# Kernel tuning notes

Hardware: AMD Instinct MI355X
Metric: run time of the kernel (lower is better)

Reference implementation:

```python
import jax, jax.numpy as jnp
import numpy as np

D_MODEL = 1024
N_HEADS = 16
D_K = D_MODEL // N_HEADS
THETA = 10000.0
B, S = 4, 2048


def setup_inputs() -> dict:
    key = jax.random.key(0)
    ks = jax.random.split(key, 5)
    scale = 0.02
    return {
        "x": jax.random.normal(ks[0], (B, S, D_MODEL), dtype=jnp.float32),
        "token_positions": jnp.arange(S, dtype=jnp.int32),
        "WQ": jax.random.normal(ks[1], (D_MODEL, D_MODEL), dtype=jnp.float32) * scale,
        "WK": jax.random.normal(ks[2], (D_MODEL, D_MODEL), dtype=jnp.float32) * scale,
        "WV": jax.random.normal(ks[3], (D_MODEL, D_MODEL), dtype=jnp.float32) * scale,
        "WO": jax.random.normal(ks[4], (D_MODEL, D_MODEL), dtype=jnp.float32) * scale,
    }


def apply_rope(x, positions):
    # x: [B, H, S, d_k]; rotate interleaved (even, odd) pairs
    half = D_K // 2
    inv_freq = THETA ** (-jnp.arange(half, dtype=x.dtype) * 2.0 / D_K)  # [half]
    ang = positions.astype(x.dtype)[:, None] * inv_freq[None, :]        # [S, half]
    cos, sin = jnp.cos(ang), jnp.sin(ang)
    x1 = x[..., 0::2]
    x2 = x[..., 1::2]
    r1 = x1 * cos - x2 * sin
    r2 = x1 * sin + x2 * cos
    return jnp.stack([r1, r2], axis=-1).reshape(x.shape)


def reference(x, token_positions, WQ, WK, WV, WO):
    b, s, _ = x.shape
    # Linear (no bias), weight stored (out, in): y = x @ W^T
    def proj(W):
        y = jnp.einsum('bsd,ed->bse', x, W)
        return y.reshape(b, s, N_HEADS, D_K).transpose(0, 2, 1, 3)  # [b,h,s,dk]
    Q, K, V = proj(WQ), proj(WK), proj(WV)
    Q = apply_rope(Q, token_positions)
    K = apply_rope(K, token_positions)
    scores = jnp.einsum('bhqd,bhkd->bhqk', Q, K) / jnp.sqrt(jnp.asarray(D_K, x.dtype))
    causal = jnp.tril(jnp.ones((s, s), dtype=bool))
    scores = jnp.where(causal, scores, -jnp.inf)
    attn = jax.nn.softmax(scores, axis=-1)
    out = jnp.einsum('bhqk,bhkd->bhqd', attn, V)
    out = out.transpose(0, 2, 1, 3).reshape(b, s, D_MODEL)
    return jnp.einsum('bse,de->bsd', out, WO)
```

## Files before the change

kernel.cpp:

```cpp
#include <hip/hip_runtime.h>
#include <cstdint>
#include <cstddef>

#define DM 1024
#define NH 16
#define DKD 64
#define BB 4
#define SS 2048
#define MTOT (BB*SS)

typedef float  f32x4  __attribute__((ext_vector_type(4)));
typedef __bf16 bf16x8 __attribute__((ext_vector_type(8)));
typedef __bf16 bf16x4v __attribute__((ext_vector_type(4)));
typedef __bf16 bf16x2v __attribute__((ext_vector_type(2)));
using as3v = __attribute__((address_space(3))) void;
using as1v = __attribute__((address_space(1))) void;

__device__ __forceinline__ void gl2lds16(const void* g, void* l) {
  __builtin_amdgcn_global_load_lds((as1v*)g, (as3v*)l, 16, 0, 0);
}

__device__ __forceinline__ float fast_exp2(float x) {
#if __has_builtin(__builtin_amdgcn_exp2f)
  return __builtin_amdgcn_exp2f(x);
#else
  return __expf(x * 0.6931471805599453f);
#endif
}

__device__ __forceinline__ void sincos_rev(float rev, float* s, float* c) {
#if __has_builtin(__builtin_amdgcn_sinf) && __has_builtin(__builtin_amdgcn_cosf)
  *s = __builtin_amdgcn_sinf(rev);
  *c = __builtin_amdgcn_cosf(rev);
#else
  float a = rev * 6.283185307179586f;
  *s = __sinf(a); *c = __cosf(a);
#endif
}

__device__ __forceinline__ uint32_t pkbf(float a, float b) {
  union { uint32_t u; __bf16 h[2]; } c;
  c.h[0] = (__bf16)a; c.h[1] = (__bf16)b;
  return c.u;
}

__global__ void cast_all_k(const float* __restrict__ x,
                           const float* __restrict__ wq, const float* __restrict__ wk,
                           const float* __restrict__ wv, const float* __restrict__ wo,
                           __bf16* __restrict__ xb,
                           __bf16* __restrict__ wqb, __bf16* __restrict__ wkb,
                           __bf16* __restrict__ wvb, __bf16* __restrict__ wob) {
  int i = blockIdx.x * blockDim.x + threadIdx.x;
  const float* src;
  __bf16* dst;
  int idx, oidx;
  if (i < 2097152) {
    src = x; dst = xb; idx = i; oidx = i;
  } else {
    int j = i - 2097152;
    int w = j >> 18;
    idx = j & 262143;
    src = (w == 0) ? wq : (w == 1) ? wk : (w == 2) ? wv : wo;
    dst = (w == 0) ? wqb : (w == 1) ? wkb : (w == 2) ? wvb : wob;
    if (w < 2) {
      int e = idx >> 8;
      int c = idx & 255;
      int d = e & 63;
      int dp = (d & 1) ? 32 + (d >> 1) : (d >> 1);
      oidx = (((e & ~63) | dp) << 8) | c;
    } else {
      oidx = idx;
    }
  }
  float4 f = ((const float4*)src)[idx];
  bf16x4v o;
  o[0] = (__bf16)f.x; o[1] = (__bf16)f.y; o[2] = (__bf16)f.z; o[3] = (__bf16)f.w;
  ((bf16x4v*)dst)[oidx] = o;
}

__global__ void rope_tbl_k(const int* __restrict__ pos, float2* __restrict__ tbl) {
  int p = blockIdx.x * blockDim.x + threadIdx.x;
  int s = p >> 5;
  int i = p & 31;
  float ps = (float)pos[s];
  float invr = __expf(-0.28782313663f * (float)i) * 0.15915494309f;
  float rev = ps * invr;
  rev -= floorf(rev);
  float sn, cs;
  sincos_rev(rev, &sn, &cs);
  tbl[p] = make_float2(cs, sn);
}

template <typename CT>
__global__ __launch_bounds__(256) void gemm_bt_k(const __bf16* __restrict__ A,
                                                 const __bf16* __restrict__ B,
                                                 CT* __restrict__ C,
                                                 int M, int N, int K) {
  __shared__ __bf16 As[128 * 32];
  __shared__ __bf16 Bs[128 * 32];
  const int tid  = threadIdx.x;
  const int lane = tid & 63;
  const int wid  = tid >> 6;
  const int lrow = lane & 15;
  const int quad = lane >> 4;
  const int m0 = blockIdx.y * 128;
  const int n0 = blockIdx.x * 128;
  const int wm = (wid & 1) * 64;
  const int wn = (wid >> 1) * 64;
  const int srow = wid * 32 + (lane >> 2);
  const int scol = (lane & 3) * 8;

  f32x4 acc[4][4] = {};

  for (int k0 = 0; k0 < K; k0 += 32) {
    __syncthreads();
    gl2lds16(A + (size_t)(m0 + srow)      * K + k0 + scol, As + (wid * 32)      * 32);
    gl2lds16(A + (size_t)(m0 + srow + 16) * K + k0 + scol, As + (wid * 32 + 16) * 32);
    gl2lds16(B + (size_t)(n0 + srow)      * K + k0 + scol, Bs + (wid * 32)      * 32);
    gl2lds16(B + (size_t)(n0 + srow + 16) * K + k0 + scol, Bs + (wid * 32 + 16) * 32);
    __syncthreads();

    bf16x8 af[4], bfr[4];
#pragma unroll
    for (int i = 0; i < 4; ++i)
      af[i] = *(const bf16x8*)(As + (wm + i * 16 + lrow) * 32 + quad * 8);
#pragma unroll
    for (int i = 0; i < 4; ++i)
      bfr[i] = *(const bf16x8*)(Bs + (wn + i * 16 + lrow) * 32 + quad * 8);
#pragma unroll
    for (int mi = 0; mi < 4; ++mi)
#pragma unroll
      for (int ni = 0; ni < 4; ++ni)
        acc[mi][ni] = __builtin_amdgcn_mfma_f32_16x16x32_bf16(af[mi], bfr[ni], acc[mi][ni], 0, 0, 0);
  }

#pragma unroll
  for (int mi = 0; mi < 4; ++mi)
#pragma unroll
    for (int ni = 0; ni < 4; ++ni)
#pragma unroll
      for (int r = 0; r < 4; ++r) {
        int row = m0 + wm + mi * 16 + quad * 4 + r;
        int col = n0 + wn + ni * 16 + lrow;
        C[(size_t)row * N + col] = (CT)acc[mi][ni][r];
      }
}

__global__ __launch_bounds__(256) void gemm_qkv_k(const __bf16* __restrict__ A,
                                                  const __bf16* __restrict__ Bq,
                                                  const __bf16* __restrict__ Bk,
                                                  const __bf16* __restrict__ Bv,
                                                  const float2* __restrict__ tbl,
                                                  __bf16* __restrict__ Cq,
                                                  __bf16* __restrict__ Ck,
                                                  __bf16* __restrict__ Cv) {
  __shared__ __bf16 As[128 * 32];
  __shared__ __bf16 Bs[128 * 32];
  const int sel = blockIdx.x >> 3;
  const __bf16* B = sel == 0 ? Bq : sel == 1 ? Bk : Bv;
  const int n0 = (blockIdx.x & 7) * 128;
  const int m0 = blockIdx.y * 128;
  const int K = DM;
  const int tid  = threadIdx.x;
  const int lane = tid & 63;
  const int wid  = tid >> 6;
  const int lrow = lane & 15;
  const int quad = lane >> 4;
  const int wm = (wid & 1) * 64;
  const int wn = (wid >> 1) * 64;
  const int srow = wid * 32 + (lane >> 2);
  const int scol = (lane & 3) * 8;

  f32x4 acc[4][4] = {};

  for (int k0 = 0; k0 < K; k0 += 32) {
    __syncthreads();
    gl2lds16(A + (size_t)(m0 + srow)      * K + k0 + scol, As + (wid * 32)      * 32);
    gl2lds16(A + (size_t)(m0 + srow + 16) * K + k0 + scol, As + (wid * 32 + 16) * 32);
    gl2lds16(B + (size_t)(n0 + srow)      * K + k0 + scol, Bs + (wid * 32)      * 32);
    gl2lds16(B + (size_t)(n0 + srow + 16) * K + k0 + scol, Bs + (wid * 32 + 16) * 32);
    __syncthreads();

    bf16x8 af[4], bfr[4];
#pragma unroll
    for (int i = 0; i < 4; ++i)
      af[i] = *(const bf16x8*)(As + (wm + i * 16 + lrow) * 32 + quad * 8);
#pragma unroll
    for (int i = 0; i < 4; ++i)
      bfr[i] = *(const bf16x8*)(Bs + (wn + i * 16 + lrow) * 32 + quad * 8);
#pragma unroll
    for (int mi = 0; mi < 4; ++mi)
#pragma unroll
      for (int ni = 0; ni < 4; ++ni)
        acc[mi][ni] = __builtin_amdgcn_mfma_f32_16x16x32_bf16(af[mi], bfr[ni], acc[mi][ni], 0, 0, 0);
  }

  const int hbase = (n0 + wn) >> 6;
  const int bq = m0 >> 11;

  if (sel == 2) {
    __bf16* vt = Cv + ((size_t)(bq * NH + hbase)) * (DKD * SS);
    const int S0 = (m0 + wm) & (SS - 1);
#pragma unroll
    for (int ni = 0; ni < 4; ++ni) {
      const int d = ni * 16 + lrow;
#pragma unroll
      for (int mi = 0; mi < 4; ++mi) {
        bf16x4v pk;
#pragma unroll
        for (int r = 0; r < 4; ++r) pk[r] = (__bf16)acc[mi][ni][r];
        const int sp = S0 + (mi >> 1) * 32 + quad * 8 + (mi & 1) * 4;
        *(bf16x4v*)(vt + (size_t)d * SS + sp) = pk;
      }
    }
  } else {
    __bf16* C = ((sel == 0) ? Cq : Ck) + ((size_t)(bq * NH + hbase)) * (SS * DKD);
#pragma unroll
    for (int ni = 0; ni < 2; ++ni) {
      const int i = ni * 16 + lrow;
#pragma unroll
      for (int mi = 0; mi < 4; ++mi) {
#pragma unroll
        for (int r = 0; r < 4; ++r) {
          int s = (m0 + wm + mi * 16 + quad * 4 + r) & (SS - 1);
          float2 cssn = tbl[s * 32 + i];
          float a = acc[mi][ni][r];
          float b = acc[mi][ni + 2][r];
          C[(size_t)s * DKD + i]      = (__bf16)fmaf(a, cssn.x, -(b * cssn.y));
          C[(size_t)s * DKD + 32 + i] = (__bf16)fmaf(a, cssn.y,  (b * cssn.x));
        }
      }
    }
  }
}

__global__ __launch_bounds__(512, 4) void attn10_k(const __bf16* __restrict__ Qh,
                                                   const __bf16* __restrict__ Kh,
                                                   const __bf16* __restrict__ VT,
                                                   __bf16* __restrict__ O) {
  __shared__ __bf16 Ks[2][128 * 64];
  __shared__ __bf16 Vt[2][64 * 128];
  const int tid  = threadIdx.x;
  const int lane = tid & 63;
  const int wid  = tid >> 6;
  const int lrow = lane & 15;
  const int quad = lane >> 4;
  const int j   = blockIdx.x;
  const int xcd = j & 7;
  const int t   = j >> 3;
  const int bh  = (xcd << 3) | (t >> 3);
  const int pr  = t & 7;
  const int qa  = pr;
  const int qb  = 15 - pr;
  const int na  = qa + 1;
  const int b  = bh >> 4;
  const int h  = bh & 15;
  const size_t hb = (size_t)bh * (SS * DKD);

  const int skr = lane >> 3;
  const int skc = lane & 7;
  const int svd = lane >> 4;
  const int svc = lane & 15;

  auto stage = [&](int kt, int bsel) {
#pragma unroll
    for (int ii = 0; ii < 2; ++ii) {
      int i = wid * 2 + ii;
      int key = i * 8 + skr;
      int gc = skc ^ (key & 7);
      gl2lds16(Kh + hb + (size_t)(kt * 128 + key) * DKD + gc * 8, &Ks[bsel][i * 512]);
      int dk = i * 4 + svd;
      int gc2 = (svc & 8) | ((svc ^ dk) & 7);
      gl2lds16(VT + hb + (size_t)dk * SS + kt * 128 + gc2 * 8, &Vt[bsel][i * 512]);
    }
  };

  stage(0, 0);
  int it = 0;

  for (int seg = 0; seg < 2; ++seg) {
    const int qi  = seg ? qb : qa;
    const int q0  = qi * 128;
    const int nkt = qi + 1;
    const int qg  = q0 + wid * 16 + lrow;

    bf16x8 qf0, qf1;
    {
      const __bf16* qp = Qh + hb + (size_t)qg * DKD + quad * 8;
      qf0 = *(const bf16x8*)qp;
      qf1 = *(const bf16x8*)(qp + 32);
    }
    f32x4 Oa[4] = {};
    float la = 0.f, lb = 0.f;

    for (int kt = 0; kt < nkt; ++kt, ++it) {
      __syncthreads();
      {
        int nit = it + 1;
        if (nit < 17) {
          int nk = (nit < na) ? nit : (nit - na);
          stage(nk, nit & 1);
        }
      }
      const __bf16* ks = Ks[it & 1];
      const __bf16* vt = Vt[it & 1];

      f32x4 sa[8];
#pragma unroll
      for (int mi = 0; mi < 8; ++mi) sa[mi] = (f32x4){0.f, 0.f, 0.f, 0.f};
      __builtin_amdgcn_s_setprio(1);
#pragma unroll
      for (int tt = 0; tt < 2; ++tt) {
        bf16x8 qf = tt ? qf1 : qf0;
#pragma unroll
        for (int mi = 0; mi < 8; ++mi) {
          bf16x8 kf = *(const bf16x8*)(ks + (mi * 16 + lrow) * 64 + (((tt * 4 + quad) ^ (lrow & 7)) * 8));
          sa[mi] = __builtin_amdgcn_mfma_f32_16x16x32_bf16(kf, qf, sa[mi], 0, 0, 0);
        }
      }
      __builtin_amdgcn_s_setprio(0);

      const bool lastt = (kt == nkt - 1);
#pragma unroll
      for (int kc = 0; kc < 4; ++kc) {
        union { uint32_t u[4]; bf16x8 v; } P;
#pragma unroll
        for (int half = 0; half < 2; ++half) {
          const int mi = kc * 2 + half;
          float pr4[4];
#pragma unroll
          for (int r = 0; r < 4; ++r) {
            float p = fast_exp2(sa[mi][r] * 0.18033688f - 8.0f);
            if (lastt) {
              int key = kt * 128 + kc * 32 + half * 16 + quad * 4 + r;
              p = (key <= qg) ? p : 0.f;
            }
            pr4[r] = p;
          }
          float s01 = pr4[0] + pr4[1];
          float s23 = pr4[2] + pr4[3];
          if (half) lb += (s01 + s23); else la += (s01 + s23);
          P.u[half * 2]     = pkbf(pr4[0], pr4[1]);
          P.u[half * 2 + 1] = pkbf(pr4[2], pr4[3]);
        }
        __builtin_amdgcn_s_setprio(1);
#pragma unroll
        for (int ni = 0; ni < 4; ++ni) {
          int c = kc * 4 + quad;
          int cp = (c & 8) | ((c ^ (lrow & 7)) & 7);
          bf16x8 vf = *(const bf16x8*)(vt + (ni * 16 + lrow) * 128 + cp * 8);
          Oa[ni] = __builtin_amdgcn_mfma_f32_16x16x32_bf16(P.v, vf, Oa[ni], 0, 0, 0);
        }
        __builtin_amdgcn_s_setprio(0);
      }
    }

    float l = la + lb;
    l += __shfl_xor(l, 16, 64);
    l += __shfl_xor(l, 32, 64);
#pragma unroll
    for (int r = 0; r < 4; ++r) {
      float li = __shfl(l, quad * 4 + r, 64);
      float inv = 1.0f / li;
      int row = q0 + wid * 16 + quad * 4 + r;
#pragma unroll
      for (int ni = 0; ni < 4; ++ni)
        O[(size_t)b * SS * DM + (size_t)row * DM + h * DKD + ni * 16 + lrow] =
            (__bf16)(Oa[ni][r] * inv);
    }
  }
}

extern "C" void kernel_launch(void* const* d_in, const int* in_sizes, int n_in,
                              void* d_out, int out_size, void* d_ws, size_t ws_size,
                              hipStream_t stream) {
  (void)in_sizes; (void)n_in; (void)out_size; (void)ws_size;
  const float* x  = (const float*)d_in[0];
  const int*   pos = (const int*)d_in[1];
  const float* WQ = (const float*)d_in[2];
  const float* WK = (const float*)d_in[3];
  const float* WV = (const float*)d_in[4];
  const float* WO = (const float*)d_in[5];
  float* out = (float*)d_out;

  char* w = (char*)d_ws;
  const size_t MB = 1024 * 1024;
  __bf16* xb  = (__bf16*)(w);
  __bf16* wqb = (__bf16*)(w + 16 * MB);
  __bf16* wkb = (__bf16*)(w + 18 * MB);
  __bf16* wvb = (__bf16*)(w + 20 * MB);
  __bf16* wob = (__bf16*)(w + 22 * MB);
  __bf16* Qh  = (__bf16*)(w + 24 * MB);
  __bf16* Kh  = (__bf16*)(w + 40 * MB);
  __bf16* Cb  = (__bf16*)(w + 56 * MB);
  __bf16* VT  = (__bf16*)(w + 72 * MB);
  float2* tbl = (float2*)(w + 88 * MB);

  cast_all_k<<<3145728 / 256, 256, 0, stream>>>(x, WQ, WK, WV, WO, xb, wqb, wkb, wvb, wob);

  rope_tbl_k<<<(SS * 32) / 256, 256, 0, stream>>>(pos, tbl);

  gemm_qkv_k<<<dim3(24, MTOT / 128), 256, 0, stream>>>(xb, wqb, wkb, wvb, tbl, Qh, Kh, VT);

  attn10_k<<<dim3(512), 512, 0, stream>>>(Qh, Kh, VT, Cb);

  gemm_bt_k<float><<<dim3(DM / 128, MTOT / 128), 256, 0, stream>>>(Cb, wob, out, MTOT, DM, DM);
}
```

Before: 256.1 us.

## Double-buffer LDS tiles with XOR swizzle and MFMA priority in GEMM kernels

Both the generic GEMM and the fused QKV GEMM now keep two LDS buffers. The next K-tile's global-to-LDS loads are issued right after a single barrier, so they overlap the MFMA work on the current tile instead of stalling behind two barriers per iteration. The LDS tile layout is XOR-swizzled across pairs of rows to cut bank conflicts on the fragment reads. s_setprio is raised around the MFMA block, and launch bounds request 4 blocks per SM. The trade-off is double the LDS footprint per block and more index arithmetic, which could limit occupancy.

```diff
diff --git a/kernel.cpp b/kernel.cpp
--- a/kernel.cpp
+++ b/kernel.cpp
@@ -91,13 +91,14 @@
   tbl[p] = make_float2(cs, sn);
 }
 
+
 template <typename CT>
-__global__ __launch_bounds__(256) void gemm_bt_k(const __bf16* __restrict__ A,
-                                                 const __bf16* __restrict__ B,
-                                                 CT* __restrict__ C,
-                                                 int M, int N, int K) {
-  __shared__ __bf16 As[128 * 32];
-  __shared__ __bf16 Bs[128 * 32];
+__global__ __launch_bounds__(256, 4) void gemm_bt_k(const __bf16* __restrict__ A,
+                                                    const __bf16* __restrict__ B,
+                                                    CT* __restrict__ C,
+                                                    int M, int N, int K) {
+  __shared__ __bf16 As[2][128 * 32];
+  __shared__ __bf16 Bs[2][128 * 32];
   const int tid  = threadIdx.x;
   const int lane = tid & 63;
   const int wid  = tid >> 6;
@@ -107,31 +108,46 @@
   const int n0 = blockIdx.x * 128;
   const int wm = (wid & 1) * 64;
   const int wn = (wid >> 1) * 64;
-  const int srow = wid * 32 + (lane >> 2);
-  const int scol = (lane & 3) * 8;
+
+  const int r0 = wid * 32 + (lane >> 2);
+  const int cs = (((r0 & 1) << 2) | (lane & 3)) ^ ((r0 >> 1) & 7);
+  const int gr = (r0 & ~1) | (cs >> 2);
+  const int gc = cs & 3;
+  const __bf16* Asrc = A + (size_t)(m0 + gr) * K + gc * 8;
+  const __bf16* Bsrc = B + (size_t)(n0 + gr) * K + gc * 8;
+  const int clf = (((lrow & 1) << 2) + quad) ^ (lrow >> 1);
 
   f32x4 acc[4][4] = {};
 
-  for (int k0 = 0; k0 < K; k0 += 32) {
+  auto stage = [&](int buf, int k0) {
+    gl2lds16(Asrc + k0,                   &As[buf][(wid * 32)      * 32]);
+    gl2lds16(Asrc + (size_t)16 * K + k0,  &As[buf][(wid * 32 + 16) * 32]);
+    gl2lds16(Bsrc + k0,                   &Bs[buf][(wid * 32)      * 32]);
+    gl2lds16(Bsrc + (size_t)16 * K + k0,  &Bs[buf][(wid * 32 + 16) * 32]);
+  };
+
+  stage(0, 0);
+  const int kiters = K >> 5;
+  for (int kk = 0; kk < kiters; ++kk) {
     __syncthreads();
-    gl2lds16(A + (size_t)(m0 + srow)      * K + k0 + scol, As + (wid * 32)      * 32);
-    gl2lds16(A + (size_t)(m0 + srow + 16) * K + k0 + scol, As + (wid * 32 + 16) * 32);
-    gl2lds16(B + (size_t)(n0 + srow)      * K + k0 + scol, Bs + (wid * 32)      * 32);
-    gl2lds16(B + (size_t)(n0 + srow + 16) * K + k0 + scol, Bs + (wid * 32 + 16) * 32);
-    __syncthreads();
+    if (kk + 1 < kiters) stage((kk + 1) & 1, (kk + 1) * 32);
+    const __bf16* as = As[kk & 1];
+    const __bf16* bs = Bs[kk & 1];
 
     bf16x8 af[4], bfr[4];
 #pragma unroll
     for (int i = 0; i < 4; ++i)
-      af[i] = *(const bf16x8*)(As + (wm + i * 16 + lrow) * 32 + quad * 8);
+      af[i] = *(const bf16x8*)(as + ((wm + i * 16 + lrow) >> 1) * 64 + clf * 8);
 #pragma unroll
     for (int i = 0; i < 4; ++i)
-      bfr[i] = *(const bf16x8*)(Bs + (wn + i * 16 + lrow) * 32 + quad * 8);
+      bfr[i] = *(const bf16x8*)(bs + ((wn + i * 16 + lrow) >> 1) * 64 + clf * 8);
+    __builtin_amdgcn_s_setprio(1);
 #pragma unroll
     for (int mi = 0; mi < 4; ++mi)
 #pragma unroll
       for (int ni = 0; ni < 4; ++ni)
         acc[mi][ni] = __builtin_amdgcn_mfma_f32_16x16x32_bf16(af[mi], bfr[ni], acc[mi][ni], 0, 0, 0);
+    __builtin_amdgcn_s_setprio(0);
   }
 
 #pragma unroll
@@ -146,16 +162,16 @@
       }
 }
 
-__global__ __launch_bounds__(256) void gemm_qkv_k(const __bf16* __restrict__ A,
-                                                  const __bf16* __restrict__ Bq,
-                                                  const __bf16* __restrict__ Bk,
-                                                  const __bf16* __restrict__ Bv,
-                                                  const float2* __restrict__ tbl,
-                                                  __bf16* __restrict__ Cq,
-                                                  __bf16* __restrict__ Ck,
-                                                  __bf16* __restrict__ Cv) {
-  __shared__ __bf16 As[128 * 32];
-  __shared__ __bf16 Bs[128 * 32];
+__global__ __launch_bounds__(256, 4) void gemm_qkv_k(const __bf16* __restrict__ A,
+                                                     const __bf16* __restrict__ Bq,
+                                                     const __bf16* __restrict__ Bk,
+                                                     const __bf16* __restrict__ Bv,
+                                                     const float2* __restrict__ tbl,
+                                                     __bf16* __restrict__ Cq,
+                                                     __bf16* __restrict__ Ck,
+                                                     __bf16* __restrict__ Cv) {
+  __shared__ __bf16 As[2][128 * 32];
+  __shared__ __bf16 Bs[2][128 * 32];
   const int sel = blockIdx.x >> 3;
   const __bf16* B = sel == 0 ? Bq : sel == 1 ? Bk : Bv;
   const int n0 = (blockIdx.x & 7) * 128;
@@ -168,31 +184,46 @@
   const int quad = lane >> 4;
   const int wm = (wid & 1) * 64;
   const int wn = (wid >> 1) * 64;
-  const int srow = wid * 32 + (lane >> 2);
-  const int scol = (lane & 3) * 8;
+
+  const int r0 = wid * 32 + (lane >> 2);
+  const int cs = (((r0 & 1) << 2) | (lane & 3)) ^ ((r0 >> 1) & 7);
+  const int gr = (r0 & ~1) | (cs >> 2);
+  const int gc = cs & 3;
+  const __bf16* Asrc = A + (size_t)(m0 + gr) * K + gc * 8;
+  const __bf16* Bsrc = B + (size_t)(n0 + gr) * K + gc * 8;
+  const int clf = (((lrow & 1) << 2) + quad) ^ (lrow >> 1);
 
   f32x4 acc[4][4] = {};
 
-  for (int k0 = 0; k0 < K; k0 += 32) {
+  auto stage = [&](int buf, int k0) {
+    gl2lds16(Asrc + k0,                   &As[buf][(wid * 32)      * 32]);
+    gl2lds16(Asrc + (size_t)16 * K + k0,  &As[buf][(wid * 32 + 16) * 32]);
+    gl2lds16(Bsrc + k0,                   &Bs[buf][(wid * 32)      * 32]);
+    gl2lds16(Bsrc + (size_t)16 * K + k0,  &Bs[buf][(wid * 32 + 16) * 32]);
+  };
+
+  stage(0, 0);
+  const int kiters = K >> 5;
+  for (int kk = 0; kk < kiters; ++kk) {
     __syncthreads();
-    gl2lds16(A + (size_t)(m0 + srow)      * K + k0 + scol, As + (wid * 32)      * 32);
-    gl2lds16(A + (size_t)(m0 + srow + 16) * K + k0 + scol, As + (wid * 32 + 16) * 32);
-    gl2lds16(B + (size_t)(n0 + srow)      * K + k0 + scol, Bs + (wid * 32)      * 32);
-    gl2lds16(B + (size_t)(n0 + srow + 16) * K + k0 + scol, Bs + (wid * 32 + 16) * 32);
-    __syncthreads();
+    if (kk + 1 < kiters) stage((kk + 1) & 1, (kk + 1) * 32);
+    const __bf16* as = As[kk & 1];
+    const __bf16* bs = Bs[kk & 1];
 
     bf16x8 af[4], bfr[4];
 #pragma unroll
     for (int i = 0; i < 4; ++i)
-      af[i] = *(const bf16x8*)(As + (wm + i * 16 + lrow) * 32 + quad * 8);
+      af[i] = *(const bf16x8*)(as + ((wm + i * 16 + lrow) >> 1) * 64 + clf * 8);
 #pragma unroll
     for (int i = 0; i < 4; ++i)
-      bfr[i] = *(const bf16x8*)(Bs + (wn + i * 16 + lrow) * 32 + quad * 8);
+      bfr[i] = *(const bf16x8*)(bs + ((wn + i * 16 + lrow) >> 1) * 64 + clf * 8);
+    __builtin_amdgcn_s_setprio(1);
 #pragma unroll
     for (int mi = 0; mi < 4; ++mi)
 #pragma unroll
       for (int ni = 0; ni < 4; ++ni)
         acc[mi][ni] = __builtin_amdgcn_mfma_f32_16x16x32_bf16(af[mi], bfr[ni], acc[mi][ni], 0, 0, 0);
+    __builtin_amdgcn_s_setprio(0);
   }
 
   const int hbase = (n0 + wn) >> 6;
```

New measurement: 260.5 us. No clear change (+1.7%).
